# Performance work log

Measured on AMD Instinct MI355X. Metric: run time of the kernel, lower is better.

The kernel has to match this reference:

```python
import jax, jax.numpy as jnp
import numpy as np

N = 20000      # nodes (atoms)
E = 200000     # directed edges
T = 800000     # triplets
H = 128        # hidden_channels
INT = 64       # int_emb_size
BAS = 8        # basis_emb_size
NS = 7         # num_spherical
NR = 6         # num_radial
OUT = 256      # out_emb_channels
NB = 4         # num_blocks
L = 3          # num_output_layers
CUT = 5.0      # cutoff
silu = jax.nn.silu  # 'swish' activation

# Envelope with exponent=5 -> p=6
_P = 6.0
_A = -(_P + 1.0) * (_P + 2.0) / 2.0   # -28
_B = _P * (_P + 2.0)                  # 48
_C = -_P * (_P + 1.0) / 2.0           # -21

def _envelope(d):
    d5 = d ** 5
    return (1.0 / d + _A * d5 + _B * d5 * d + _C * d5 * d * d) * (d < 1.0).astype(d.dtype)

def setup_inputs() -> dict:
    key = jax.random.key(0)
    ks = iter(jax.random.split(key, 64))
    def p(shape, scale=0.05):
        return jax.random.normal(next(ks), shape, dtype=jnp.float32) * scale
    inp = {}
    inp['z'] = jax.random.randint(next(ks), (N,), 0, 95)
    inp['dist'] = jax.random.uniform(next(ks), (E,), minval=0.1, maxval=CUT, dtype=jnp.float32)
    inp['sbf'] = p((T, NS * NR), 1.0)
    inp['i'] = jax.random.randint(next(ks), (E,), 0, N)
    inp['j'] = jax.random.randint(next(ks), (E,), 0, N)
    inp['idx_kj'] = jax.random.randint(next(ks), (T,), 0, E)
    inp['idx_ji'] = jax.random.randint(next(ks), (T,), 0, E)
    # embedding block params
    s3 = float(np.sqrt(3.0))
    inp['emb_table'] = jax.random.uniform(next(ks), (95, H), minval=-s3, maxval=s3, dtype=jnp.float32)
    inp['W_rbf_emb'] = p((NR, H)); inp['b_rbf_emb'] = jnp.zeros((H,), jnp.float32)
    inp['W_emb'] = p((3 * H, H)); inp['b_emb'] = jnp.zeros((H,), jnp.float32)
    inp['freq'] = jnp.arange(1, NR + 1, dtype=jnp.float32) * jnp.pi
    # interaction blocks (stacked over NB)
    inp['Wi_rbf1'] = p((NB, NR, BAS)); inp['Wi_rbf2'] = p((NB, BAS, H))
    inp['Wi_sbf1'] = p((NB, NS * NR, BAS)); inp['Wi_sbf2'] = p((NB, BAS, INT))
    inp['Wi_kj'] = p((NB, H, H)); inp['bi_kj'] = jnp.zeros((NB, H), jnp.float32)
    inp['Wi_ji'] = p((NB, H, H)); inp['bi_ji'] = jnp.zeros((NB, H), jnp.float32)
    inp['Wi_down'] = p((NB, H, INT)); inp['Wi_up'] = p((NB, INT, H))
    inp['Wi_rb_W1'] = p((NB, H, H)); inp['Wi_rb_b1'] = jnp.zeros((NB, H), jnp.float32)
    inp['Wi_rb_W2'] = p((NB, H, H)); inp['Wi_rb_b2'] = jnp.zeros((NB, H), jnp.float32)
    inp['Wi_lin'] = p((NB, H, H)); inp['bi_lin'] = jnp.zeros((NB, H), jnp.float32)
    inp['Wi_ra_W1'] = p((NB, H, H)); inp['Wi_ra_b1'] = jnp.zeros((NB, H), jnp.float32)
    inp['Wi_ra_W2'] = p((NB, H, H)); inp['Wi_ra_b2'] = jnp.zeros((NB, H), jnp.float32)
    # output blocks (stacked over NB+1)
    inp['Wo_rbf'] = p((NB + 1, NR, H)); inp['Wo_up'] = p((NB + 1, H, OUT))
    inp['Wo_linW'] = p((NB + 1, L, OUT, OUT)); inp['Wo_linb'] = jnp.zeros((NB + 1, L, OUT), jnp.float32)
    return inp

def _forward(z, dist, sbf, i, j, idx_kj, idx_ji,
             emb_table, W_rbf_emb, b_rbf_emb, W_emb, b_emb, freq,
             Wi_rbf1, Wi_rbf2, Wi_sbf1, Wi_sbf2, Wi_kj, bi_kj, Wi_ji, bi_ji,
             Wi_down, Wi_up, Wi_rb_W1, Wi_rb_b1, Wi_rb_W2, Wi_rb_b2,
             Wi_lin, bi_lin, Wi_ra_W1, Wi_ra_b1, Wi_ra_W2, Wi_ra_b2,
             Wo_rbf, Wo_up, Wo_linW, Wo_linb):
    num_nodes = z.shape[0]
    num_edges = dist.shape[0]
    # BesselBasisLayer: rbf [E, NR]
    d = dist / CUT
    rbf = _envelope(d)[:, None] * jnp.sin(freq * d[:, None])
    # EmbeddingBlock -> edge features x [E, H]
    h = emb_table[z]
    rbf_h = silu(rbf @ W_rbf_emb + b_rbf_emb)
    x = silu(jnp.concatenate([h[i], h[j], rbf_h], axis=-1) @ W_emb + b_emb)

    def out_block(b, x_e):
        t = (rbf @ Wo_rbf[b]) * x_e                      # [E, H]
        node = jax.ops.segment_sum(t, i, num_segments=num_nodes)
        node = node @ Wo_up[b]                            # [N, OUT]
        for l in range(L):
            node = silu(node @ Wo_linW[b, l] + Wo_linb[b, l])
        return node

    P = out_block(0, x)
    for b in range(NB):
        # InteractionPPBlock
        x_ji = silu(x @ Wi_ji[b] + bi_ji[b])
        x_kj = silu(x @ Wi_kj[b] + bi_kj[b])
        rbf_b = (rbf @ Wi_rbf1[b]) @ Wi_rbf2[b]           # [E, H]
        x_kj = x_kj * rbf_b
        x_kj = silu(x_kj @ Wi_down[b])                    # [E, INT]
        sbf_b = (sbf @ Wi_sbf1[b]) @ Wi_sbf2[b]           # [T, INT]
        x_kj = x_kj[idx_kj] * sbf_b                       # gather triplets
        x_kj = jax.ops.segment_sum(x_kj, idx_ji, num_segments=num_edges)
        x_kj = silu(x_kj @ Wi_up[b])                      # [E, H]
        hdd = x_ji + x_kj
        # one residual layer before skip (num_before_skip=1)
        hdd = hdd + silu(silu(hdd @ Wi_rb_W1[b] + Wi_rb_b1[b]) @ Wi_rb_W2[b] + Wi_rb_b2[b])
        hdd = silu(hdd @ Wi_lin[b] + bi_lin[b]) + x
        # one residual layer after skip (source uses num_before_skip here too)
        hdd = hdd + silu(silu(hdd @ Wi_ra_W1[b] + Wi_ra_b1[b]) @ Wi_ra_W2[b] + Wi_ra_b2[b])
        x = hdd
        P = P + out_block(b + 1, x)
    return P  # [N, OUT] per-node output embeddings

def reference(z, dist, sbf, i, j, idx_kj, idx_ji,
              emb_table, W_rbf_emb, b_rbf_emb, W_emb, b_emb, freq,
              Wi_rbf1, Wi_rbf2, Wi_sbf1, Wi_sbf2, Wi_kj, bi_kj, Wi_ji, bi_ji,
              Wi_down, Wi_up, Wi_rb_W1, Wi_rb_b1, Wi_rb_W2, Wi_rb_b2,
              Wi_lin, bi_lin, Wi_ra_W1, Wi_ra_b1, Wi_ra_W2, Wi_ra_b2,
              Wo_rbf, Wo_up, Wo_linW, Wo_linb):
    return _forward(z, dist, sbf, i, j, idx_kj, idx_ji,
                    emb_table, W_rbf_emb, b_rbf_emb, W_emb, b_emb, freq,
                    Wi_rbf1, Wi_rbf2, Wi_sbf1, Wi_sbf2, Wi_kj, bi_kj, Wi_ji, bi_ji,
                    Wi_down, Wi_up, Wi_rb_W1, Wi_rb_b1, Wi_rb_W2, Wi_rb_b2,
                    Wi_lin, bi_lin, Wi_ra_W1, Wi_ra_b1, Wi_ra_W2, Wi_ra_b2,
                    Wo_rbf, Wo_up, Wo_linW, Wo_linb)
```

## Files before the change

### kernel.cpp

```cpp
#include <hip/hip_runtime.h>
#include <hip/hip_bf16.h>

#define NND 20000
#define NE  200000
#define NT  800000

#define SW256(row) (((row) & 7) << 4)
#define SW128(row) (((row) & 7) << 4)

typedef short  s16x8 __attribute__((ext_vector_type(8)));
typedef float  f32x4 __attribute__((ext_vector_type(4)));

__device__ __forceinline__ float silu_f(float v) {
    return v * __builtin_amdgcn_rcpf(1.0f + __expf(-v));
}

__device__ __forceinline__ ushort f2bf(float f) {
    uint u = __float_as_uint(f);
    uint r = (u + 0x7FFFu + ((u >> 16) & 1u)) >> 16;
    return (ushort)r;
}
__device__ __forceinline__ float bf2f(ushort u) {
    return __uint_as_float(((uint)u) << 16);
}
__device__ __forceinline__ uint f2bf_pk(float a, float b) {
    __hip_bfloat162 h = __float22bfloat162_rn(make_float2(a, b));
    return *(uint*)&h;
}
__device__ __forceinline__ void store_bf4(void* p, float v0, float v1, float v2, float v3) {
    uint2 o;
    o.x = f2bf_pk(v0, v1);
    o.y = f2bf_pk(v2, v3);
    *(uint2*)p = o;
}

__global__ void rbf_kernel(const float* __restrict__ dist, const float* __restrict__ freq,
                           float* __restrict__ rbf, int E)
{
    int e = blockIdx.x * blockDim.x + threadIdx.x;
    if (e >= E) return;
    float d = dist[e] * 0.2f;
    float d5 = d * d; d5 = d5 * d5 * d;
    float env = 1.0f / d + (-28.0f) * d5 + 48.0f * d5 * d + (-21.0f) * d5 * d * d;
    env = (d < 1.0f) ? env : 0.0f;
    float fr[6];
    #pragma unroll
    for (int r = 0; r < 6; ++r) fr[r] = freq[r];
    #pragma unroll
    for (int r = 0; r < 6; ++r)
        rbf[(size_t)e * 6 + r] = env * sinf(fr[r] * d);
}

__global__ void twt_kernel(const float* __restrict__ W, ushort* __restrict__ Wt,
                           int CIN, int COUT, int total)
{
    int idx = blockIdx.x * 256 + threadIdx.x;
    if (idx >= total) return;
    int per = CIN * COUT;
    int b = idx / per, r = idx % per;
    int k = r / COUT, c = r % COUT;
    Wt[(size_t)b * per + (size_t)c * CIN + k] = f2bf(W[idx]);
}

__global__ void twt7_kernel(const float* __restrict__ s0, const float* __restrict__ s1,
                            const float* __restrict__ s2, const float* __restrict__ s3,
                            const float* __restrict__ s4, const float* __restrict__ s5,
                            const float* __restrict__ s6, ushort* __restrict__ dst)
{
    int idx = blockIdx.x * 256 + threadIdx.x;
    int which = idx >> 16;
    int r = idx & 65535;
    const float* s = (which == 0) ? s0 : (which == 1) ? s1 : (which == 2) ? s2 :
                     (which == 3) ? s3 : (which == 4) ? s4 : (which == 5) ? s5 : s6;
    int b = r >> 14;
    int rr = r & 16383;
    int k = rr >> 7, c = rr & 127;
    dst[(size_t)which * 65536 + b * 16384 + c * 128 + k] = f2bf(s[r]);
}

__global__ void cvt_sbf_kernel(const float* __restrict__ in, ushort* __restrict__ out, int total4)
{
    int idx = blockIdx.x * 256 + threadIdx.x;
    if (idx >= total4) return;
    float4 f = *(const float4*)(in + (size_t)idx * 4);
    ushort4 o;
    o.x = f2bf(f.x); o.y = f2bf(f.y); o.z = f2bf(f.z); o.w = f2bf(f.w);
    *(ushort4*)(out + (size_t)idx * 4) = o;
}

template<int CIN, int COUT, int MODE, typename IT, typename ET, typename OT>
__global__ __launch_bounds__(256) void mfma_lin_kernel(
    const IT* __restrict__ x, const ushort* __restrict__ Wt,
    const float* __restrict__ bias, const ET* __restrict__ extra,
    OT* __restrict__ y, int M)
{
    constexpr int MT = 64;
    constexpr int NF = COUT / 16;
    constexpr int KS = CIN / 32;
    constexpr int PITCH = CIN * 2;
    __shared__ ushort As_u[MT * CIN];
    __shared__ ushort Ws_u[COUT * CIN];
    char* As = (char*)As_u;
    char* Ws = (char*)Ws_u;
    const int tid = threadIdx.x;
    const int row0 = blockIdx.x * MT;
    const bool full = (row0 + MT <= M);

    constexpr int ACH = MT * CIN / 8;
    for (int c = tid; c < ACH; c += 256) {
        int row = c / (CIN / 8);
        int kc  = c % (CIN / 8);
        int grow = row0 + row;
        s16x8 v;
        if (full || grow < M) {
            if constexpr (sizeof(IT) == 4) {
                const float* src = (const float*)x + (size_t)grow * CIN + kc * 8;
                float4 f0 = *(const float4*)(src);
                float4 f1 = *(const float4*)(src + 4);
                v[0] = (short)f2bf(f0.x); v[1] = (short)f2bf(f0.y);
                v[2] = (short)f2bf(f0.z); v[3] = (short)f2bf(f0.w);
                v[4] = (short)f2bf(f1.x); v[5] = (short)f2bf(f1.y);
                v[6] = (short)f2bf(f1.z); v[7] = (short)f2bf(f1.w);
            } else {
                v = *(const s16x8*)((const ushort*)x + (size_t)grow * CIN + kc * 8);
            }
        } else {
            #pragma unroll
            for (int u = 0; u < 8; ++u) v[u] = 0;
        }
        *(s16x8*)(As + ((row * PITCH + kc * 16) ^ SW256(row))) = v;
    }
    constexpr int WCH = COUT * CIN / 8;
    for (int c = tid; c < WCH; c += 256) {
        int col = c / (CIN / 8);
        int kc  = c % (CIN / 8);
        s16x8 v = *(const s16x8*)(Wt + (size_t)col * CIN + kc * 8);
        *(s16x8*)(Ws + ((col * PITCH + kc * 16) ^ SW256(col))) = v;
    }
    __syncthreads();

    const int w = tid >> 6, lane = tid & 63;
    const int l15 = lane & 15, l4 = lane >> 4;
    const int arow = w * 16 + l15;

    f32x4 acc[NF];
    #pragma unroll
    for (int nf = 0; nf < NF; ++nf) acc[nf] = (f32x4){0.f, 0.f, 0.f, 0.f};

    #pragma unroll
    for (int ks = 0; ks < KS; ++ks) {
        const int kbyte = (ks * 32 + l4 * 8) * 2;
        s16x8 a = *(const s16x8*)(As + ((arow * PITCH + kbyte) ^ SW256(arow)));
        #pragma unroll
        for (int nf = 0; nf < NF; ++nf) {
            int col = nf * 16 + l15;
            s16x8 bf = *(const s16x8*)(Ws + ((col * PITCH + kbyte) ^ SW256(col)));
            acc[nf] = __builtin_amdgcn_mfma_f32_16x16x32_bf16(bf, a, acc[nf], 0, 0, 0);
        }
    }

    const int grow = row0 + w * 16 + l15;
    if (grow < M) {
        #pragma unroll
        for (int nf = 0; nf < NF; ++nf) {
            int c0 = nf * 16 + l4 * 4;
            float4 bv = make_float4(0.f, 0.f, 0.f, 0.f);
            if (bias) bv = *(const float4*)(bias + c0);
            float v0 = acc[nf][0] + bv.x, v1 = acc[nf][1] + bv.y;
            float v2 = acc[nf][2] + bv.z, v3 = acc[nf][3] + bv.w;
            if constexpr (MODE & 1) {
                v0 = silu_f(v0); v1 = silu_f(v1); v2 = silu_f(v2); v3 = silu_f(v3);
            }
            if constexpr ((MODE & 4) != 0) {
                if constexpr (sizeof(ET) == 4) {
                    float4 ex = *(const float4*)((const float*)extra + (size_t)grow * COUT + c0);
                    v0 += ex.x; v1 += ex.y; v2 += ex.z; v3 += ex.w;
                } else {
                    ushort4 ex = *(const ushort4*)((const ushort*)extra + (size_t)grow * COUT + c0);
                    v0 += bf2f(ex.x); v1 += bf2f(ex.y); v2 += bf2f(ex.z); v3 += bf2f(ex.w);
                }
            }
            if constexpr (sizeof(OT) == 4) {
                float* o = (float*)y + (size_t)grow * COUT + c0;
                if constexpr (MODE & 8) {
                    float4 cur = *(const float4*)o;
                    v0 += cur.x; v1 += cur.y; v2 += cur.z; v3 += cur.w;
                }
                *(float4*)o = make_float4(v0, v1, v2, v3);
            } else {
                store_bf4((ushort*)y + (size_t)grow * COUT + c0, v0, v1, v2, v3);
            }
        }
    }
}

__global__ __launch_bounds__(256) void mfma_front_kernel(
    const ushort* __restrict__ x,
    const ushort* __restrict__ Wt1, const ushort* __restrict__ Wt2,
    const ushort* __restrict__ Wtd,
    const float* __restrict__ b1, const float* __restrict__ b2,
    const float* __restrict__ rbf, const float* __restrict__ W1r,
    const float* __restrict__ W2r,
    ushort* __restrict__ y1, ushort* __restrict__ yd, int M)
{
    constexpr int PITCH = 256;
    __shared__ ushort A_u[64 * 128];
    __shared__ ushort W1_u[128 * 128];
    __shared__ ushort W2_u[128 * 128];
    char* A = (char*)A_u;
    char* W1s = (char*)W1_u;
    char* W2s = (char*)W2_u;
    const int tid = threadIdx.x;
    const int row0 = blockIdx.x * 64;

    for (int c = tid; c < 1024; c += 256) {
        int row = c >> 4, kc = c & 15;
        s16x8 v = *(const s16x8*)(x + (size_t)(row0 + row) * 128 + kc * 8);
        *(s16x8*)(A + ((row * PITCH + kc * 16) ^ SW256(row))) = v;
    }
    for (int c = tid; c < 2048; c += 256) {
        int col = c >> 4, kc = c & 15;
        int o = (col * PITCH + kc * 16) ^ SW256(col);
        *(s16x8*)(W1s + o) = *(const s16x8*)(Wt1 + (size_t)col * 128 + kc * 8);
        *(s16x8*)(W2s + o) = *(const s16x8*)(Wt2 + (size_t)col * 128 + kc * 8);
    }
    s16x8 wdreg[4];
    #pragma unroll
    for (int i = 0; i < 4; ++i) {
        int c = tid + i * 256;
        wdreg[i] = *(const s16x8*)(Wtd + (size_t)(c >> 4) * 128 + (c & 15) * 8);
    }
    __syncthreads();

    const int w = tid >> 6, lane = tid & 63;
    const int l15 = lane & 15, l4 = lane >> 4;
    const int arow = w * 16 + l15;

    f32x4 acc1[8], acc2[8];
    #pragma unroll
    for (int nf = 0; nf < 8; ++nf) {
        acc1[nf] = (f32x4){0.f, 0.f, 0.f, 0.f};
        acc2[nf] = (f32x4){0.f, 0.f, 0.f, 0.f};
    }
    #pragma unroll
    for (int ks = 0; ks < 4; ++ks) {
        const int kbyte = (ks * 32 + l4 * 8) * 2;
        s16x8 a = *(const s16x8*)(A + ((arow * PITCH + kbyte) ^ SW256(arow)));
        #pragma unroll
        for (int nf = 0; nf < 8; ++nf) {
            int col = nf * 16 + l15;
            int o = (col * PITCH + kbyte) ^ SW256(col);
            s16x8 bf1 = *(const s16x8*)(W1s + o);
            s16x8 bf2 = *(const s16x8*)(W2s + o);
            acc1[nf] = __builtin_amdgcn_mfma_f32_16x16x32_bf16(bf1, a, acc1[nf], 0, 0, 0);
            acc2[nf] = __builtin_amdgcn_mfma_f32_16x16x32_bf16(bf2, a, acc2[nf], 0, 0, 0);
        }
    }
    __syncthreads();

    const int grow = row0 + arow;
    float rv[6];
    #pragma unroll
    for (int q = 0; q < 6; ++q) rv[q] = rbf[(size_t)grow * 6 + q];
    float t8[8];
    #pragma unroll
    for (int p = 0; p < 8; ++p) {
        float s = 0.f;
        #pragma unroll
        for (int q = 0; q < 6; ++q) s += rv[q] * W1r[q * 8 + p];
        t8[p] = s;
    }
    #pragma unroll
    for (int nf = 0; nf < 8; ++nf) {
        int c0 = nf * 16 + l4 * 4;
        float4 bb1 = *(const float4*)(b1 + c0);
        float4 bb2 = *(const float4*)(b2 + c0);
        store_bf4(y1 + (size_t)grow * 128 + c0,
                  silu_f(acc1[nf][0] + bb1.x), silu_f(acc1[nf][1] + bb1.y),
                  silu_f(acc1[nf][2] + bb1.z), silu_f(acc1[nf][3] + bb1.w));
        float r0 = 0.f, r1 = 0.f, r2 = 0.f, r3 = 0.f;
        #pragma unroll
        for (int p = 0; p < 8; ++p) {
            float4 wq = *(const float4*)(W2r + p * 128 + c0);
            float tp = t8[p];
            r0 += tp * wq.x; r1 += tp * wq.y; r2 += tp * wq.z; r3 += tp * wq.w;
        }
        store_bf4(A + ((arow * PITCH + c0 * 2) ^ SW256(arow)),
                  silu_f(acc2[nf][0] + bb2.x) * r0, silu_f(acc2[nf][1] + bb2.y) * r1,
                  silu_f(acc2[nf][2] + bb2.z) * r2, silu_f(acc2[nf][3] + bb2.w) * r3);
    }
    #pragma unroll
    for (int i = 0; i < 4; ++i) {
        int c = tid + i * 256;
        int col = c >> 4, kc = c & 15;
        *(s16x8*)(W1s + ((col * PITCH + kc * 16) ^ SW256(col))) = wdreg[i];
    }
    __syncthreads();

    f32x4 accd[4];
    #pragma unroll
    for (int nf = 0; nf < 4; ++nf) accd[nf] = (f32x4){0.f, 0.f, 0.f, 0.f};
    #pragma unroll
    for (int ks = 0; ks < 4; ++ks) {
        const int kbyte = (ks * 32 + l4 * 8) * 2;
        s16x8 a = *(const s16x8*)(A + ((arow * PITCH + kbyte) ^ SW256(arow)));
        #pragma unroll
        for (int nf = 0; nf < 4; ++nf) {
            int col = nf * 16 + l15;
            s16x8 bf = *(const s16x8*)(W1s + ((col * PITCH + kbyte) ^ SW256(col)));
            accd[nf] = __builtin_amdgcn_mfma_f32_16x16x32_bf16(bf, a, accd[nf], 0, 0, 0);
        }
    }
    #pragma unroll
    for (int nf = 0; nf < 4; ++nf) {
        int c0 = nf * 16 + l4 * 4;
        store_bf4(yd + (size_t)grow * 64 + c0,
                  silu_f(accd[nf][0]), silu_f(accd[nf][1]),
                  silu_f(accd[nf][2]), silu_f(accd[nf][3]));
    }
}

__global__ __launch_bounds__(256) void mfma_back_kernel(
    const ushort* __restrict__ go, const ushort* __restrict__ xji,
    const ushort* __restrict__ x,
    const ushort* __restrict__ Wup, const ushort* __restrict__ Wrb1,
    const ushort* __restrict__ Wrb2, const ushort* __restrict__ Wlin,
    const ushort* __restrict__ Wra1, const ushort* __restrict__ Wra2,
    const float* __restrict__ b_rb1, const float* __restrict__ b_rb2,
    const float* __restrict__ b_lin, const float* __restrict__ b_ra1,
    const float* __restrict__ b_ra2,
    ushort* __restrict__ xout, int M)
{
    __shared__ ushort A_u[64 * 128];
    __shared__ ushort T_u[64 * 128];
    char* A  = (char*)A_u;
    char* Tb = (char*)T_u;
    const int tid = threadIdx.x;
    const int row0 = blockIdx.x * 64;
    const int w = tid >> 6, lane = tid & 63;
    const int l15 = lane & 15, l4 = lane >> 4;
    const int colbase = w * 32;

    f32x4 acc[8];
    s16x8 wfA[8], wfB[8];
    ushort4 xr[8];

    auto zero_acc = [&]() {
        #pragma unroll
        for (int i = 0; i < 8; ++i) acc[i] = (f32x4){0.f, 0.f, 0.f, 0.f};
    };
    auto load_w8 = [&](s16x8* wf, const ushort* Wg) {
        #pragma unroll
        for (int nfi = 0; nfi < 2; ++nfi)
            #pragma unroll
            for (int ks = 0; ks < 4; ++ks)
                wf[nfi * 4 + ks] = *(const s16x8*)(
                    Wg + (size_t)(colbase + nfi * 16 + l15) * 128 + ks * 32 + l4 * 8);
    };
    auto load_rows = [&](const ushort* src) {
        #pragma unroll
        for (int rt = 0; rt < 4; ++rt) {
            int grow = row0 + rt * 16 + l15;
            #pragma unroll
            for (int nfi = 0; nfi < 2; ++nfi) {
                int c0 = colbase + nfi * 16 + l4 * 4;
                xr[rt * 2 + nfi] = *(const ushort4*)(src + (size_t)grow * 128 + c0);
            }
        }
    };
    auto run_phase = [&](char* Ab, const s16x8* wf) {
        #pragma unroll
        for (int rt = 0; rt < 4; ++rt) {
            int row = rt * 16 + l15;
            #pragma unroll
            for (int ks = 0; ks < 4; ++ks) {
                s16x8 a = *(const s16x8*)(Ab + ((row * 256 + ks * 64 + l4 * 16) ^ SW256(row)));
                acc[rt * 2 + 0] = __builtin_amdgcn_mfma_f32_16x16x32_bf16(wf[0 * 4 + ks], a, acc[rt * 2 + 0], 0, 0, 0);
                acc[rt * 2 + 1] = __builtin_amdgcn_mfma_f32_16x16x32_bf16(wf[1 * 4 + ks], a, acc[rt * 2 + 1], 0, 0, 0);
            }
        }
    };

    s16x8 wfUp[4];
    #pragma unroll
    for (int nfi = 0; nfi < 2; ++nfi)
        #pragma unroll
        for (int ks = 0; ks < 2; ++ks)
            wfUp[nfi * 2 + ks] = *(const s16x8*)(
                Wup + (size_t)(colbase + nfi * 16 + l15) * 64 + ks * 32 + l4 * 8);
    for (int c = tid; c < 512; c += 256) {
        int row = c >> 3, kc = c & 7;
        s16x8 v = *(const s16x8*)(go + (size_t)(row0 + row) * 64 + kc * 8);
        *(s16x8*)(Tb + ((row * 128 + kc * 16) ^ SW128(row))) = v;
    }
    load_w8(wfA, Wrb1);
    load_rows(xji);
    __syncthreads();

    zero_acc();
    #pragma unroll
    for (int rt = 0; rt < 4; ++rt) {
        int row = rt * 16 + l15;
        #pragma unroll
        for (int ks = 0; ks < 2; ++ks) {
            s16x8 a = *(const s16x8*)(Tb + ((row * 128 + ks * 64 + l4 * 16) ^ SW128(row)));
            acc[rt * 2 + 0] = __builtin_amdgcn_mfma_f32_16x16x32_bf16(wfUp[0 * 2 + ks], a, acc[rt * 2 + 0], 0, 0, 0);
            acc[rt * 2 + 1] = __builtin_amdgcn_mfma_f32_16x16x32_bf16(wfUp[1 * 2 + ks], a, acc[rt * 2 + 1], 0, 0, 0);
        }
    }
    #pragma unroll
    for (int rt = 0; rt < 4; ++rt) {
        int row = rt * 16 + l15;
        #pragma unroll
        for (int nfi = 0; nfi < 2; ++nfi) {
            int c0 = colbase + nfi * 16 + l4 * 4;
            f32x4 v = acc[rt * 2 + nfi];
            ushort4 xj = xr[rt * 2 + nfi];
            store_bf4(A + ((row * 256 + c0 * 2) ^ SW256(row)),
                      bf2f(xj.x) + silu_f(v[0]), bf2f(xj.y) + silu_f(v[1]),
                      bf2f(xj.z) + silu_f(v[2]), bf2f(xj.w) + silu_f(v[3]));
        }
    }
    __syncthreads();

    load_w8(wfB, Wrb2);
    zero_acc();
    run_phase(A, wfA);
    #pragma unroll
    for (int rt = 0; rt < 4; ++rt) {
        int row = rt * 16 + l15;
        #pragma unroll
        for (int nfi = 0; nfi < 2; ++nfi) {
            int c0 = colbase + nfi * 16 + l4 * 4;
            f32x4 v = acc[rt * 2 + nfi];
            float4 bb = *(const float4*)(b_rb1 + c0);
            store_bf4(Tb + ((row * 256 + c0 * 2) ^ SW256(row)),
                      silu_f(v[0] + bb.x), silu_f(v[1] + bb.y),
                      silu_f(v[2] + bb.z), silu_f(v[3] + bb.w));
        }
    }
    __syncthreads();

    load_w8(wfA, Wlin);
    load_rows(x);
    zero_acc();
    run_phase(Tb, wfB);
    #pragma unroll
    for (int rt = 0; rt < 4; ++rt) {
        int row = rt * 16 + l15;
        #pragma unroll
        for (int nfi = 0; nfi < 2; ++nfi) {
            int c0 = colbase + nfi * 16 + l4 * 4;
            f32x4 v = acc[rt * 2 + nfi];
            float4 bb = *(const float4*)(b_rb2 + c0);
            int ao = (row * 256 + c0 * 2) ^ SW256(row);
            ushort4 h = *(const ushort4*)(A + ao);
            store_bf4(A + ao,
                      bf2f(h.x) + silu_f(v[0] + bb.x), bf2f(h.y) + silu_f(v[1] + bb.y),
                      bf2f(h.z) + silu_f(v[2] + bb.z), bf2f(h.w) + silu_f(v[3] + bb.w));
        }
    }
    __syncthreads();

    load_w8(wfB, Wra1);
    zero_acc();
    run_phase(A, wfA);
    __syncthreads();
    #pragma unroll
    for (int rt = 0; rt < 4; ++rt) {
        int row = rt * 16 + l15;
        #pragma unroll
        for (int nfi = 0; nfi < 2; ++nfi) {
            int c0 = colbase + nfi * 16 + l4 * 4;
            f32x4 v = acc[rt * 2 + nfi];
            float4 bb = *(const float4*)(b_lin + c0);
            ushort4 xv = xr[rt * 2 + nfi];
            store_bf4(A + ((row * 256 + c0 * 2) ^ SW256(row)),
                      silu_f(v[0] + bb.x) + bf2f(xv.x), silu_f(v[1] + bb.y) + bf2f(xv.y),
                      silu_f(v[2] + bb.z) + bf2f(xv.z), silu_f(v[3] + bb.w) + bf2f(xv.w));
        }
    }
    __syncthreads();

    load_w8(wfA, Wra2);
    zero_acc();
    run_phase(A, wfB);
    #pragma unroll
    for (int rt = 0; rt < 4; ++rt) {
        int row = rt * 16 + l15;
        #pragma unroll
        for (int nfi = 0; nfi < 2; ++nfi) {
            int c0 = colbase + nfi * 16 + l4 * 4;
            f32x4 v = acc[rt * 2 + nfi];
            float4 bb = *(const float4*)(b_ra1 + c0);
            store_bf4(Tb + ((row * 256 + c0 * 2) ^ SW256(row)),
                      silu_f(v[0] + bb.x), silu_f(v[1] + bb.y),
                      silu_f(v[2] + bb.z), silu_f(v[3] + bb.w));
        }
    }
    __syncthreads();

    zero_acc();
    run_phase(Tb, wfA);
    #pragma unroll
    for (int rt = 0; rt < 4; ++rt) {
        int row = rt * 16 + l15;
        int grow = row0 + row;
        #pragma unroll
        for (int nfi = 0; nfi < 2; ++nfi) {
            int c0 = colbase + nfi * 16 + l4 * 4;
            f32x4 v = acc[rt * 2 + nfi];
            float4 bb = *(const float4*)(b_ra2 + c0);
            ushort4 h = *(const ushort4*)(A + ((row * 256 + c0 * 2) ^ SW256(row)));
            store_bf4(xout + (size_t)grow * 128 + c0,
                      bf2f(h.x) + silu_f(v[0] + bb.x), bf2f(h.y) + silu_f(v[1] + bb.y),
                      bf2f(h.z) + silu_f(v[2] + bb.z), bf2f(h.w) + silu_f(v[3] + bb.w));
        }
    }
}

__global__ __launch_bounds__(256) void node_gather_kernel(
    const float* __restrict__ rbf, const float* __restrict__ Wo,
    const ushort* __restrict__ x, const int* __restrict__ noffs,
    const int* __restrict__ nedge, float* __restrict__ node, int N)
{
    const int tid = threadIdx.x;
    const int col = tid & 127;
    const int n = blockIdx.x * 2 + (tid >> 7);
    if (n >= N) return;
    float wo[6];
    #pragma unroll
    for (int q = 0; q < 6; ++q) wo[q] = Wo[q * 128 + col];
    float acc = 0.f;
    const int k0 = noffs[n], k1 = noffs[n + 1];
    for (int k = k0; k < k1; ++k) {
        int e = nedge[k];
        const float* rb = rbf + (size_t)e * 6;
        float t = wo[0] * rb[0] + wo[1] * rb[1] + wo[2] * rb[2]
                + wo[3] * rb[3] + wo[4] * rb[4] + wo[5] * rb[5];
        acc += t * bf2f(x[(size_t)e * 128 + col]);
    }
    node[(size_t)n * 128 + col] = acc;
}

__global__ __launch_bounds__(256) void mfma_out_kernel(
    const float* __restrict__ node,
    const ushort* __restrict__ Wup, const ushort* __restrict__ Wlin,
    const float* __restrict__ BL, float* __restrict__ P, int N)
{
    __shared__ ushort A_u[64 * 256];
    __shared__ ushort T_u[64 * 256];
    __shared__ ushort W_u[128 * 128];
    char* A  = (char*)A_u;
    char* Tb = (char*)T_u;
    char* Ws = (char*)W_u;
    const int tid = threadIdx.x;
    const int row0 = blockIdx.x * 64;
    const int w = tid >> 6, lane = tid & 63;
    const int l15 = lane & 15, l4 = lane >> 4;
    const int arow = w * 16 + l15;
    const int grow = row0 + arow;
    const int c_base = l4 * 4;

    f32x4 acc[16];
    s16x8 wreg[8];

    auto prefetch_w = [&](const ushort* base, int stride) {
        #pragma unroll
        for (int i = 0; i < 8; ++i) {
            int c = tid + i * 256;
            int col = c >> 4, kc = c & 15;
            wreg[i] = *(const s16x8*)(base + (size_t)col * stride + kc * 8);
        }
    };
    auto commit_w = [&]() {
        #pragma unroll
        for (int i = 0; i < 8; ++i) {
            int c = tid + i * 256;
            int col = c >> 4, kc = c & 15;
            *(s16x8*)(Ws + ((col * 256 + kc * 16) ^ SW256(col))) = wreg[i];
        }
    };
    auto run8 = [&](char* Ab, int apitch, int kboff, int accoff) {
        #pragma unroll
        for (int ks = 0; ks < 4; ++ks) {
            const int kbw = ks * 64 + l4 * 16;
            s16x8 a = *(const s16x8*)(Ab + ((arow * apitch + kboff + kbw) ^ SW256(arow)));
            #pragma unroll
            for (int nf = 0; nf < 8; ++nf) {
                int col = nf * 16 + l15;
                s16x8 bf = *(const s16x8*)(Ws + ((col * 256 + kbw) ^ SW256(col)));
                acc[accoff + nf] = __builtin_amdgcn_mfma_f32_16x16x32_bf16(bf, a, acc[accoff + nf], 0, 0, 0);
            }
        }
    };

    #pragma unroll
    for (int i = 0; i < 16; ++i) acc[i] = (f32x4){0.f, 0.f, 0.f, 0.f};

    for (int c = tid; c < 1024; c += 256) {
        int row = c >> 4, kc = c & 15;
        int gr = row0 + row;
        s16x8 v;
        if (gr < N) {
            const float* src = node + (size_t)gr * 128 + kc * 8;
            float4 f0 = *(const float4*)src;
            float4 f1 = *(const float4*)(src + 4);
            v[0] = (short)f2bf(f0.x); v[1] = (short)f2bf(f0.y);
            v[2] = (short)f2bf(f0.z); v[3] = (short)f2bf(f0.w);
            v[4] = (short)f2bf(f1.x); v[5] = (short)f2bf(f1.y);
            v[6] = (short)f2bf(f1.z); v[7] = (short)f2bf(f1.w);
        } else {
            #pragma unroll
            for (int u = 0; u < 8; ++u) v[u] = 0;
        }
        *(s16x8*)(Tb + ((row * 256 + kc * 16) ^ SW256(row))) = v;
    }
    prefetch_w(Wup, 128);
    __syncthreads();
    commit_w();
    prefetch_w(Wup + 128 * 128, 128);
    __syncthreads();
    run8(Tb, 256, 0, 0);
    __syncthreads();
    commit_w();
    prefetch_w(Wlin, 256);
    __syncthreads();
    run8(Tb, 256, 0, 8);
    #pragma unroll
    for (int nf = 0; nf < 16; ++nf) {
        int c0 = nf * 16 + c_base;
        store_bf4(A + ((arow * 512 + c0 * 2) ^ SW256(arow)),
                  acc[nf][0], acc[nf][1], acc[nf][2], acc[nf][3]);
    }
    __syncthreads();

    char* S = A; char* D = Tb;
    for (int l = 0; l < 3; ++l) {
        #pragma unroll
        for (int i = 0; i < 16; ++i) acc[i] = (f32x4){0.f, 0.f, 0.f, 0.f};
        const ushort* WL = Wlin + (size_t)l * 65536;
        for (int q = 0; q < 4; ++q) {
            int ch = q & 1, kh = q >> 1;
            commit_w();
            if (q < 3) {
                int nq = q + 1;
                prefetch_w(WL + (size_t)(nq & 1) * 128 * 256 + (nq >> 1) * 128, 256);
            } else if (l < 2) {
                prefetch_w(Wlin + (size_t)(l + 1) * 65536, 256);
            }
            __syncthreads();
            run8(S, 512, kh * 256, ch * 8);
            __syncthreads();
        }
        const float* bl = BL + l * 256;
        if (l < 2) {
            #pragma unroll
            for (int nf = 0; nf < 16; ++nf) {
                int c0 = nf * 16 + c_base;
                float4 bb = *(const float4*)(bl + c0);
                store_bf4(D + ((arow * 512 + c0 * 2) ^ SW256(arow)),
                          silu_f(acc[nf][0] + bb.x), silu_f(acc[nf][1] + bb.y),
                          silu_f(acc[nf][2] + bb.z), silu_f(acc[nf][3] + bb.w));
            }
            __syncthreads();
            char* tmp = S; S = D; D = tmp;
        } else if (grow < N) {
            #pragma unroll
            for (int nf = 0; nf < 16; ++nf) {
                int c0 = nf * 16 + c_base;
                float4 bb = *(const float4*)(bl + c0);
                float* o = P + (size_t)grow * 256 + c0;
                float4 cur = *(const float4*)o;
                *(float4*)o = make_float4(cur.x + silu_f(acc[nf][0] + bb.x),
                                          cur.y + silu_f(acc[nf][1] + bb.y),
                                          cur.z + silu_f(acc[nf][2] + bb.z),
                                          cur.w + silu_f(acc[nf][3] + bb.w));
            }
        }
    }
}

template<int CIN, int COUT, int MODE, typename OT>
__global__ __launch_bounds__(256) void lin_kernel(
    const float* __restrict__ x, const float* __restrict__ W,
    const float* __restrict__ bias, const float* __restrict__ extra,
    OT* __restrict__ y, int M)
{
    constexpr int MT = 64;
    constexpr int CG = COUT / 4;
    constexpr int RG = 256 / CG;
    constexpr int MR = MT / RG;
    __shared__ float xs[MT * CIN];

    const int row0 = blockIdx.x * MT;
    const int tid  = threadIdx.x;
    const int rem  = M - row0;

    if (rem >= MT) {
        const float4* src = (const float4*)(x + (size_t)row0 * CIN);
        constexpr int TOT4 = (MT * CIN) / 4;
        for (int idx = tid; idx < TOT4; idx += 256)
            ((float4*)xs)[idx] = src[idx];
    } else {
        for (int idx = tid; idx < MT * CIN; idx += 256) {
            int r = idx / CIN;
            xs[idx] = (r < rem) ? x[(size_t)(row0 + r) * CIN + (idx % CIN)] : 0.0f;
        }
    }
    __syncthreads();

    const int cg = tid % CG, rg = tid / CG;
    const int c0 = cg * 4;
    float acc[MR][4];
    #pragma unroll
    for (int m = 0; m < MR; ++m) { acc[m][0]=0; acc[m][1]=0; acc[m][2]=0; acc[m][3]=0; }

    for (int k = 0; k < CIN; ++k) {
        float4 w = *(const float4*)(W + (size_t)k * COUT + c0);
        #pragma unroll
        for (int m = 0; m < MR; ++m) {
            float xv = xs[(rg * MR + m) * CIN + k];
            acc[m][0] += xv * w.x; acc[m][1] += xv * w.y;
            acc[m][2] += xv * w.z; acc[m][3] += xv * w.w;
        }
    }

    float4 bv = make_float4(0.f, 0.f, 0.f, 0.f);
    if (bias) bv = *(const float4*)(bias + c0);

    #pragma unroll
    for (int m = 0; m < MR; ++m) {
        int row = row0 + rg * MR + m;
        if (row >= M) continue;
        float v[4] = { acc[m][0] + bv.x, acc[m][1] + bv.y, acc[m][2] + bv.z, acc[m][3] + bv.w };
        if constexpr (MODE & 1) {
            #pragma unroll
            for (int u = 0; u < 4; ++u) v[u] = silu_f(v[u]);
        }
        if constexpr (sizeof(OT) == 4) {
            *(float4*)((float*)y + (size_t)row * COUT + c0) = make_float4(v[0], v[1], v[2], v[3]);
        } else {
            store_bf4((ushort*)y + (size_t)row * COUT + c0, v[0], v[1], v[2], v[3]);
        }
    }
}

__global__ __launch_bounds__(256) void fuse_embed_kernel(
    const int* __restrict__ z, const int* __restrict__ ii, const int* __restrict__ jj,
    const float* __restrict__ pt1, const float* __restrict__ pt2,
    const ushort* __restrict__ t3, const float* __restrict__ bias,
    ushort* __restrict__ x, int E)
{
    int idx = blockIdx.x * 256 + threadIdx.x;
    int e = idx >> 5;
    if (e >= E) return;
    int c4 = (idx & 31) * 4;
    int zi = z[ii[e]], zj = z[jj[e]];
    float4 a = *(const float4*)(pt1 + zi * 128 + c4);
    float4 b = *(const float4*)(pt2 + zj * 128 + c4);
    ushort4 t = *(const ushort4*)(t3 + (size_t)e * 128 + c4);
    float4 bb = *(const float4*)(bias + c4);
    store_bf4(x + (size_t)e * 128 + c4,
              silu_f(a.x + b.x + bf2f(t.x) + bb.x), silu_f(a.y + b.y + bf2f(t.y) + bb.y),
              silu_f(a.z + b.z + bf2f(t.z) + bb.z), silu_f(a.w + b.w + bf2f(t.w) + bb.w));
}

__global__ __launch_bounds__(256) void s1_kernel(
    const ushort* __restrict__ sbf16, const float* __restrict__ W1,
    const int* __restrict__ pos, ushort* __restrict__ s1, int T)
{
    constexpr int TT = 32;
    __shared__ float s_sbf[TT][42];
    __shared__ float s_w1[42 * 8];
    __shared__ ushort s_out[TT][8];
    const int t0 = blockIdx.x * TT;
    const int tid = threadIdx.x;

    for (int k = tid; k < 42 * 8; k += 256) s_w1[k] = W1[k];
    for (int k = tid; k < TT * 42; k += 256) {
        int t = k / 42, q = k % 42;
        int gt = t0 + t;
        s_sbf[t][q] = (gt < T) ? bf2f(sbf16[(size_t)gt * 42 + q]) : 0.0f;
    }
    __syncthreads();
    {
        int t = tid >> 3, p = tid & 7;
        float s = 0.0f;
        #pragma unroll
        for (int q = 0; q < 42; ++q) s += s_sbf[t][q] * s_w1[q * 8 + p];
        s_out[t][p] = f2bf(s);
    }
    __syncthreads();
    if (tid < TT) {
        int gt = t0 + tid;
        if (gt < T)
            *(s16x8*)(s1 + (size_t)pos[gt] * 8) = *(const s16x8*)s_out[tid];
    }
}

__global__ void count_kernel(const int* __restrict__ seg, int* __restrict__ deg, int T)
{
    int t = blockIdx.x * blockDim.x + threadIdx.x;
    if (t < T) atomicAdd(&deg[seg[t]], 1);
}

__global__ __launch_bounds__(256) void scan1_kernel(const int* __restrict__ deg,
                                                    int* __restrict__ offs,
                                                    int* __restrict__ bsum, int E)
{
    __shared__ int s[256];
    int tid = threadIdx.x;
    int g = blockIdx.x * 256 + tid;
    int v = (g < E) ? deg[g] : 0;
    s[tid] = v;
    __syncthreads();
    for (int d = 1; d < 256; d <<= 1) {
        int t = (tid >= d) ? s[tid - d] : 0;
        __syncthreads();
        s[tid] += t;
        __syncthreads();
    }
    if (g < E) offs[g] = s[tid] - v;
    if (tid == 255) bsum[blockIdx.x] = s[255];
}

__global__ __launch_bounds__(1024) void scan2_kernel(int* __restrict__ bsum, int NB)
{
    __shared__ int s[1024];
    int tid = threadIdx.x;
    int v = (tid < NB) ? bsum[tid] : 0;
    s[tid] = v;
    __syncthreads();
    for (int d = 1; d < 1024; d <<= 1) {
        int t = (tid >= d) ? s[tid - d] : 0;
        __syncthreads();
        s[tid] += t;
        __syncthreads();
    }
    if (tid < NB) bsum[tid] = s[tid] - v;
}

__global__ __launch_bounds__(256) void scan3_kernel(int* __restrict__ offs,
                                                    const int* __restrict__ bsum,
                                                    int E, int T)
{
    int g = blockIdx.x * 256 + threadIdx.x;
    if (g < E) offs[g] += bsum[blockIdx.x];
    if (g == 0) offs[E] = T;
}

__global__ void fill_kernel(const int* __restrict__ idx_ji, const int* __restrict__ idx_kj,
                            const int* __restrict__ offs, int* __restrict__ cursor,
                            int* __restrict__ kj_csr, int* __restrict__ pos, int T)
{
    int t = blockIdx.x * blockDim.x + threadIdx.x;
    if (t >= T) return;
    int ji = idx_ji[t];
    int slot = atomicAdd(&cursor[ji], 1);
    int k = offs[ji] + slot;
    kj_csr[k] = idx_kj[t];
    pos[t] = k;
}

__global__ void fillN_kernel(const int* __restrict__ ii, const int* __restrict__ offs,
                             int* __restrict__ cursor, int* __restrict__ elist, int E)
{
    int e = blockIdx.x * blockDim.x + threadIdx.x;
    if (e >= E) return;
    int n = ii[e];
    int slot = atomicAdd(&cursor[n], 1);
    elist[offs[n] + slot] = e;
}

__global__ __launch_bounds__(256) void gather2_kernel(
    const ushort* __restrict__ s1, const float* __restrict__ W2,
    const ushort* __restrict__ xd, const int* __restrict__ kj_csr,
    const int* __restrict__ offs, ushort* __restrict__ out, int E)
{
    const int lane = threadIdx.x & 63;
    const int e = blockIdx.x * 4 + (threadIdx.x >> 6);
    if (e >= E) return;
    float w2[8];
    #pragma unroll
    for (int p = 0; p < 8; ++p) w2[p] = W2[p * 64 + lane];
    float accA = 0.0f, accB = 0.0f;
    const int k0 = offs[e], k1 = offs[e + 1];
    int k = k0;
    for (; k + 1 < k1; k += 2) {
        s16x8 sv0 = *(const s16x8*)(s1 + (size_t)k * 8);
        s16x8 sv1 = *(const s16x8*)(s1 + (size_t)(k + 1) * 8);
        int kj0 = kj_csr[k];
        int kj1 = kj_csr[k + 1];
        float x0 = bf2f(xd[(size_t)kj0 * 64 + lane]);
        float x1 = bf2f(xd[(size_t)kj1 * 64 + lane]);
        float sb0 = bf2f((ushort)sv0[0]) * w2[0] + bf2f((ushort)sv0[1]) * w2[1]
                  + bf2f((ushort)sv0[2]) * w2[2] + bf2f((ushort)sv0[3]) * w2[3]
                  + bf2f((ushort)sv0[4]) * w2[4] + bf2f((ushort)sv0[5]) * w2[5]
                  + bf2f((ushort)sv0[6]) * w2[6] + bf2f((ushort)sv0[7]) * w2[7];
        float sb1 = bf2f((ushort)sv1[0]) * w2[0] + bf2f((ushort)sv1[1]) * w2[1]
                  + bf2f((ushort)sv1[2]) * w2[2] + bf2f((ushort)sv1[3]) * w2[3]
                  + bf2f((ushort)sv1[4]) * w2[4] + bf2f((ushort)sv1[5]) * w2[5]
                  + bf2f((ushort)sv1[6]) * w2[6] + bf2f((ushort)sv1[7]) * w2[7];
        accA += sb0 * x0;
        accB += sb1 * x1;
    }
    if (k < k1) {
        s16x8 sv = *(const s16x8*)(s1 + (size_t)k * 8);
        int kj = kj_csr[k];
        float sb = bf2f((ushort)sv[0]) * w2[0] + bf2f((ushort)sv[1]) * w2[1]
                 + bf2f((ushort)sv[2]) * w2[2] + bf2f((ushort)sv[3]) * w2[3]
                 + bf2f((ushort)sv[4]) * w2[4] + bf2f((ushort)sv[5]) * w2[5]
                 + bf2f((ushort)sv[6]) * w2[6] + bf2f((ushort)sv[7]) * w2[7];
        accA += sb * bf2f(xd[(size_t)kj * 64 + lane]);
    }
    out[(size_t)e * 64 + lane] = f2bf(accA + accB);
}

extern "C" void kernel_launch(void* const* d_in, const int* in_sizes, int n_in,
                              void* d_out, int out_size, void* d_ws, size_t ws_size,
                              hipStream_t stream)
{
    const int*   z         = (const int*)  d_in[0];
    const float* dist      = (const float*)d_in[1];
    const float* sbf       = (const float*)d_in[2];
    const int*   ii        = (const int*)  d_in[3];
    const int*   jj        = (const int*)  d_in[4];
    const int*   idx_kj    = (const int*)  d_in[5];
    const int*   idx_ji    = (const int*)  d_in[6];
    const float* emb_table = (const float*)d_in[7];
    const float* W_rbf_emb = (const float*)d_in[8];
    const float* b_rbf_emb = (const float*)d_in[9];
    const float* W_emb     = (const float*)d_in[10];
    const float* b_emb     = (const float*)d_in[11];
    const float* freq      = (const float*)d_in[12];
    const float* Wi_rbf1   = (const float*)d_in[13];
    const float* Wi_rbf2   = (const float*)d_in[14];
    const float* Wi_sbf1   = (const float*)d_in[15];
    const float* Wi_sbf2   = (const float*)d_in[16];
    const float* Wi_kj     = (const float*)d_in[17];
    const float* bi_kj     = (const float*)d_in[18];
    const float* Wi_ji     = (const float*)d_in[19];
    const float* bi_ji     = (const float*)d_in[20];
    const float* Wi_down   = (const float*)d_in[21];
    const float* Wi_up     = (const float*)d_in[22];
    const float* Wi_rb_W1  = (const float*)d_in[23];
    const float* Wi_rb_b1  = (const float*)d_in[24];
    const float* Wi_rb_W2  = (const float*)d_in[25];
    const float* Wi_rb_b2  = (const float*)d_in[26];
    const float* Wi_lin    = (const float*)d_in[27];
    const float* bi_lin    = (const float*)d_in[28];
    const float* Wi_ra_W1  = (const float*)d_in[29];
    const float* Wi_ra_b1  = (const float*)d_in[30];
    const float* Wi_ra_W2  = (const float*)d_in[31];
    const float* Wi_ra_b2  = (const float*)d_in[32];
    const float* Wo_rbf    = (const float*)d_in[33];
    const float* Wo_up     = (const float*)d_in[34];
    const float* Wo_linW   = (const float*)d_in[35];
    const float* Wo_linb   = (const float*)d_in[36];

    const int N = NND, E = NE, T = NT;
    float* ws = (float*)d_ws;
    size_t off = 0;
    float* rbf  = ws + off; off += (size_t)E * 6;
    float* buf0 = ws + off; off += (size_t)E * 128;
    float* buf1 = ws + off; off += (size_t)E * 128;
    float* buf2 = ws + off; off += (size_t)E * 128;
    float* buf3 = ws + off; off += (size_t)E * 64;
    float* buf4 = ws + off; off += (size_t)E * 64;
    int* ideg  = (int*)(ws + off); off += E;
    int* ioffs = (int*)(ws + off); off += E + 1;
    int* icur  = (int*)(ws + off); off += E;
    int* ikj   = (int*)(ws + off); off += T;
    int* ipos  = (int*)(ws + off); off += T;
    int* ibsum = (int*)(ws + off); off += 1024;
    int* ndeg  = (int*)(ws + off); off += N;
    int* noffs = (int*)(ws + off); off += N + 1;
    int* ncur  = (int*)(ws + off); off += N;
    int* nedge = (int*)(ws + off); off += E;
    int* nbsum = (int*)(ws + off); off += 1024;
    float* pt1 = ws + off; off += 95 * 128;
    float* pt2 = ws + off; off += 95 * 128;
    ushort* wt_ji   = (ushort*)(ws + off);
    ushort* wt_kj   = wt_ji   + 4 * 16384;
    ushort* wt_rb1  = wt_kj   + 4 * 16384;
    ushort* wt_rb2  = wt_rb1  + 4 * 16384;
    ushort* wt_lin  = wt_rb2  + 4 * 16384;
    ushort* wt_ra1  = wt_lin  + 4 * 16384;
    ushort* wt_ra2  = wt_ra1  + 4 * 16384;
    ushort* wt_down = wt_ra2  + 4 * 16384;
    ushort* wt_up   = wt_down + 4 * 8192;
    ushort* wt_emb3 = wt_up   + 4 * 8192;
    ushort* wt_oup  = wt_emb3 + 16384;
    ushort* wt_olin = wt_oup  + 5 * 32768;
    off += (7 * 4 * 16384 + 2 * 4 * 8192 + 16384 + 5 * 32768 + 15 * 65536 + 1) / 2;

    ushort* xb     = (ushort*)buf0;
    ushort* xjib   = (ushort*)buf1;
    ushort* rbfhb  = (ushort*)buf2;
    ushort* t3b    = (ushort*)buf1;
    ushort* s1b    = (ushort*)buf2;
    ushort* sbf16  = (ushort*)(buf2 + (size_t)4 * 1024 * 1024);
    ushort* xdb    = (ushort*)buf3;
    ushort* gob    = (ushort*)buf4;
    float*  node   = buf3;
    float* P = (float*)d_out;

    const int gridE  = (E + 63) / 64;
    const int gridN  = (N + 63) / 64;
    const int NB_SCAN  = (E + 255) / 256;
    const int NB_SCANN = (N + 255) / 256;

    hipMemsetAsync(d_out, 0, (size_t)N * 256 * 4, stream);

    twt7_kernel<<<7 * 65536 / 256, 256, 0, stream>>>(
        Wi_ji, Wi_kj, Wi_rb_W1, Wi_rb_W2, Wi_lin, Wi_ra_W1, Wi_ra_W2, wt_ji);
    twt_kernel<<<128, 256, 0, stream>>>(Wi_down,  wt_down, 128,  64, 4 * 8192);
    twt_kernel<<<128, 256, 0, stream>>>(Wi_up,    wt_up,    64, 128, 4 * 8192);
    twt_kernel<<<64,  256, 0, stream>>>(W_emb + 256 * 128, wt_emb3, 128, 128, 16384);
    twt_kernel<<<640, 256, 0, stream>>>(Wo_up,   wt_oup,  128, 256, 5 * 32768);
    twt_kernel<<<3840, 256, 0, stream>>>(Wo_linW, wt_olin, 256, 256, 15 * 65536);

    hipMemsetAsync(ideg, 0, (size_t)E * 4, stream);
    count_kernel<<<(T + 255) / 256, 256, 0, stream>>>(idx_ji, ideg, T);
    scan1_kernel<<<NB_SCAN, 256, 0, stream>>>(ideg, ioffs, ibsum, E);
    scan2_kernel<<<1, 1024, 0, stream>>>(ibsum, NB_SCAN);
    scan3_kernel<<<NB_SCAN, 256, 0, stream>>>(ioffs, ibsum, E, T);
    hipMemsetAsync(icur, 0, (size_t)E * 4, stream);
    fill_kernel<<<(T + 255) / 256, 256, 0, stream>>>(idx_ji, idx_kj, ioffs, icur, ikj, ipos, T);

    hipMemsetAsync(ndeg, 0, (size_t)N * 4, stream);
    count_kernel<<<(E + 255) / 256, 256, 0, stream>>>(ii, ndeg, E);
    scan1_kernel<<<NB_SCANN, 256, 0, stream>>>(ndeg, noffs, nbsum, N);
    scan2_kernel<<<1, 1024, 0, stream>>>(nbsum, NB_SCANN);
    scan3_kernel<<<NB_SCANN, 256, 0, stream>>>(noffs, nbsum, N, E);
    hipMemsetAsync(ncur, 0, (size_t)N * 4, stream);
    fillN_kernel<<<(E + 255) / 256, 256, 0, stream>>>(ii, noffs, ncur, nedge, E);

    rbf_kernel<<<(E + 255) / 256, 256, 0, stream>>>(dist, freq, rbf, E);
    lin_kernel<6, 128, 1, ushort><<<gridE, 256, 0, stream>>>(rbf, W_rbf_emb, b_rbf_emb, nullptr, rbfhb, E);
    lin_kernel<128, 128, 0, float><<<2, 256, 0, stream>>>(emb_table, W_emb, nullptr, nullptr, pt1, 95);
    lin_kernel<128, 128, 0, float><<<2, 256, 0, stream>>>(emb_table, W_emb + 128 * 128, nullptr, nullptr, pt2, 95);
    mfma_lin_kernel<128, 128, 0, ushort, float, ushort><<<gridE, 256, 0, stream>>>(
        rbfhb, wt_emb3, nullptr, nullptr, t3b, E);
    cvt_sbf_kernel<<<(T * 42 / 4 + 255) / 256, 256, 0, stream>>>(sbf, sbf16, T * 42 / 4);
    fuse_embed_kernel<<<(E * 32 + 255) / 256, 256, 0, stream>>>(z, ii, jj, pt1, pt2, t3b, b_emb, xb, E);

    auto out_block = [&](int b) {
        node_gather_kernel<<<(N + 1) / 2, 256, 0, stream>>>(
            rbf, Wo_rbf + (size_t)b * 6 * 128, xb, noffs, nedge, node, N);
        mfma_out_kernel<<<gridN, 256, 0, stream>>>(
            node, wt_oup + (size_t)b * 32768, wt_olin + (size_t)b * 3 * 65536,
            Wo_linb + (size_t)b * 3 * 256, P, N);
    };

    out_block(0);

    for (int b = 0; b < 4; ++b) {
        mfma_front_kernel<<<gridE, 256, 0, stream>>>(
            xb, wt_ji + (size_t)b * 16384, wt_kj + (size_t)b * 16384,
            wt_down + (size_t)b * 8192,
            bi_ji + b * 128, bi_kj + b * 128,
            rbf, Wi_rbf1 + (size_t)b * 48, Wi_rbf2 + (size_t)b * 1024,
            xjib, xdb, E);
        s1_kernel<<<(T + 31) / 32, 256, 0, stream>>>(
            sbf16, Wi_sbf1 + (size_t)b * 336, ipos, s1b, T);
        gather2_kernel<<<(E + 3) / 4, 256, 0, stream>>>(
            s1b, Wi_sbf2 + (size_t)b * 512, xdb, ikj, ioffs, gob, E);
        mfma_back_kernel<<<gridE, 256, 0, stream>>>(
            gob, xjib, xb,
            wt_up + (size_t)b * 8192, wt_rb1 + (size_t)b * 16384,
            wt_rb2 + (size_t)b * 16384, wt_lin + (size_t)b * 16384,
            wt_ra1 + (size_t)b * 16384, wt_ra2 + (size_t)b * 16384,
            Wi_rb_b1 + b * 128, Wi_rb_b2 + b * 128, bi_lin + b * 128,
            Wi_ra_b1 + b * 128, Wi_ra_b2 + b * 128,
            xb, E);

        out_block(b + 1);
    }
}
```

Before: 2.125 ms.

## Compute sbf projections for all blocks in one pass over fp32 sbf

Replaces the per-block s1 kernel and the one-time bf16 conversion of sbf with a single kernel that reads fp32 sbf once and computes the 8-wide projections for all four interaction blocks, writing them into a stacked buffer. Each block's gather then indexes its slice. This removes three repeated reads of the large triplet basis tensor and the conversion pass. It needs a larger scratch region for four sets of projections and assumes buf2 is big enough.

```diff
diff --git a/kernel.cpp b/kernel.cpp
--- a/kernel.cpp
+++ b/kernel.cpp
@@ -76,16 +76,6 @@
     int rr = r & 16383;
     int k = rr >> 7, c = rr & 127;
     dst[(size_t)which * 65536 + b * 16384 + c * 128 + k] = f2bf(s[r]);
-}
-
-__global__ void cvt_sbf_kernel(const float* __restrict__ in, ushort* __restrict__ out, int total4)
-{
-    int idx = blockIdx.x * 256 + threadIdx.x;
-    if (idx >= total4) return;
-    float4 f = *(const float4*)(in + (size_t)idx * 4);
-    ushort4 o;
-    o.x = f2bf(f.x); o.y = f2bf(f.y); o.z = f2bf(f.z); o.w = f2bf(f.w);
-    *(ushort4*)(out + (size_t)idx * 4) = o;
 }
 
 template<int CIN, int COUT, int MODE, typename IT, typename ET, typename OT>
@@ -766,36 +756,46 @@
               silu_f(a.z + b.z + bf2f(t.z) + bb.z), silu_f(a.w + b.w + bf2f(t.w) + bb.w));
 }
 
-__global__ __launch_bounds__(256) void s1_kernel(
-    const ushort* __restrict__ sbf16, const float* __restrict__ W1,
-    const int* __restrict__ pos, ushort* __restrict__ s1, int T)
+__global__ __launch_bounds__(256) void s1all_kernel(
+    const float* __restrict__ sbf, const float* __restrict__ W1,
+    const int* __restrict__ pos, ushort* __restrict__ s1all, int T)
 {
     constexpr int TT = 32;
     __shared__ float s_sbf[TT][42];
-    __shared__ float s_w1[42 * 8];
-    __shared__ ushort s_out[TT][8];
+    __shared__ float s_w1[4 * 42 * 8];
+    __shared__ ushort s_out[4][TT][8];
     const int t0 = blockIdx.x * TT;
     const int tid = threadIdx.x;
 
-    for (int k = tid; k < 42 * 8; k += 256) s_w1[k] = W1[k];
+    for (int k = tid; k < 4 * 42 * 8; k += 256) s_w1[k] = W1[k];
     for (int k = tid; k < TT * 42; k += 256) {
         int t = k / 42, q = k % 42;
         int gt = t0 + t;
-        s_sbf[t][q] = (gt < T) ? bf2f(sbf16[(size_t)gt * 42 + q]) : 0.0f;
+        s_sbf[t][q] = (gt < T) ? sbf[(size_t)gt * 42 + q] : 0.0f;
     }
     __syncthreads();
     {
         int t = tid >> 3, p = tid & 7;
-        float s = 0.0f;
-        #pragma unroll
-        for (int q = 0; q < 42; ++q) s += s_sbf[t][q] * s_w1[q * 8 + p];
-        s_out[t][p] = f2bf(s);
-    }
-    __syncthreads();
-    if (tid < TT) {
-        int gt = t0 + tid;
+        float a0 = 0.f, a1 = 0.f, a2 = 0.f, a3 = 0.f;
+        #pragma unroll
+        for (int q = 0; q < 42; ++q) {
+            float xv = s_sbf[t][q];
+            a0 += xv * s_w1[0 * 336 + q * 8 + p];
+            a1 += xv * s_w1[1 * 336 + q * 8 + p];
+            a2 += xv * s_w1[2 * 336 + q * 8 + p];
+            a3 += xv * s_w1[3 * 336 + q * 8 + p];
+        }
+        s_out[0][t][p] = f2bf(a0);
+        s_out[1][t][p] = f2bf(a1);
+        s_out[2][t][p] = f2bf(a2);
+        s_out[3][t][p] = f2bf(a3);
+    }
+    __syncthreads();
+    if (tid < 128) {
+        int b = tid >> 5, t = tid & 31;
+        int gt = t0 + t;
         if (gt < T)
-            *(s16x8*)(s1 + (size_t)pos[gt] * 8) = *(const s16x8*)s_out[tid];
+            *(s16x8*)(s1all + ((size_t)b * T + pos[gt]) * 8) = *(const s16x8*)s_out[b][t];
     }
 }
 
@@ -999,8 +999,7 @@
     ushort* xjib   = (ushort*)buf1;
     ushort* rbfhb  = (ushort*)buf2;
     ushort* t3b    = (ushort*)buf1;
-    ushort* s1b    = (ushort*)buf2;
-    ushort* sbf16  = (ushort*)(buf2 + (size_t)4 * 1024 * 1024);
+    ushort* s1all  = (ushort*)buf2;
     ushort* xdb    = (ushort*)buf3;
     ushort* gob    = (ushort*)buf4;
     float*  node   = buf3;
@@ -1043,8 +1042,8 @@
     lin_kernel<128, 128, 0, float><<<2, 256, 0, stream>>>(emb_table, W_emb + 128 * 128, nullptr, nullptr, pt2, 95);
     mfma_lin_kernel<128, 128, 0, ushort, float, ushort><<<gridE, 256, 0, stream>>>(
         rbfhb, wt_emb3, nullptr, nullptr, t3b, E);
-    cvt_sbf_kernel<<<(T * 42 / 4 + 255) / 256, 256, 0, stream>>>(sbf, sbf16, T * 42 / 4);
     fuse_embed_kernel<<<(E * 32 + 255) / 256, 256, 0, stream>>>(z, ii, jj, pt1, pt2, t3b, b_emb, xb, E);
+    s1all_kernel<<<(T + 31) / 32, 256, 0, stream>>>(sbf, Wi_sbf1, ipos, s1all, T);
 
     auto out_block = [&](int b) {
         node_gather_kernel<<<(N + 1) / 2, 256, 0, stream>>>(
@@ -1063,10 +1062,8 @@
             bi_ji + b * 128, bi_kj + b * 128,
             rbf, Wi_rbf1 + (size_t)b * 48, Wi_rbf2 + (size_t)b * 1024,
             xjib, xdb, E);
-        s1_kernel<<<(T + 31) / 32, 256, 0, stream>>>(
-            sbf16, Wi_sbf1 + (size_t)b * 336, ipos, s1b, T);
         gather2_kernel<<<(E + 3) / 4, 256, 0, stream>>>(
-            s1b, Wi_sbf2 + (size_t)b * 512, xdb, ikj, ioffs, gob, E);
+            s1all + (size_t)b * T * 8, Wi_sbf2 + (size_t)b * 512, xdb, ikj, ioffs, gob, E);
         mfma_back_kernel<<<gridE, 256, 0, stream>>>(
             gob, xjib, xb,
             wt_up + (size_t)b * 8192, wt_rb1 + (size_t)b * 16384,
```

Measured after the change: 1.979 ms. 6.9% less time.
